# Performance work log

Measured on AMD Instinct MI355X. Metric: run time of the kernel, lower is better.

## Reference

```python
import jax, jax.numpy as jnp
import numpy as np

EPS = 1e-5

def _layer_norm(y, w, b):
    mu = y.mean(-1, keepdims=True)
    var = jnp.mean((y - mu) ** 2, axis=-1, keepdims=True)
    return (y - mu) * jax.lax.rsqrt(var + EPS) * w + b


def setup_inputs() -> dict:
    key = jax.random.key(0)
    ks = jax.random.split(key, 8)
    B, D, H, W = 1, 96, 96, 96
    N, R, K = 16, 6, 4
    x = jax.random.normal(ks[0], (B, D, H, W), jnp.float32)
    x_proj_weight = jax.random.normal(ks[1], (K, R + 2 * N, D), jnp.float32) * 0.05
    dt_projs_weight = jax.random.normal(ks[2], (K, D, R), jnp.float32) * 0.1
    dt_projs_bias = jax.random.normal(ks[3], (K, D), jnp.float32) * 0.1
    A_logs = jax.random.normal(ks[4], (K * D, N), jnp.float32)
    Ds = jax.random.normal(ks[5], (K * D,), jnp.float32) * 0.1
    ln_w = jnp.ones((D,), jnp.float32)
    ln_b = jnp.zeros((D,), jnp.float32)
    return {"x": x, "x_proj_weight": x_proj_weight, "dt_projs_weight": dt_projs_weight,
            "dt_projs_bias": dt_projs_bias, "A_logs": A_logs, "Ds": Ds,
            "ln_w": ln_w, "ln_b": ln_b}


def reference(x, x_proj_weight, dt_projs_weight, dt_projs_bias, A_logs, Ds, ln_w, ln_b):
    B, D, H, W = x.shape
    L = H * W
    K = x_proj_weight.shape[0]            # 4 scan directions
    N = A_logs.shape[1]                   # d_state
    R = dt_projs_weight.shape[2]          # dt_rank

    # ---- CrossScan: 4 directional flattenings -> xs [B, K, D, L]
    xs0 = x.reshape(B, D, L)
    xs1 = jnp.swapaxes(x, 2, 3).reshape(B, D, L)
    xs = jnp.stack([xs0, xs1, xs0[:, :, ::-1], xs1[:, :, ::-1]], axis=1)

    # ---- input-dependent projections
    x_dbl = jnp.einsum('bkdl,kcd->bkcl', xs, x_proj_weight)    # [B,K,R+2N,L]
    dts = x_dbl[:, :, :R]
    Bs = x_dbl[:, :, R:R + N]                                  # [B,K,N,L]
    Cs = x_dbl[:, :, R + N:]                                   # [B,K,N,L]
    dts = jnp.einsum('bkrl,kdr->bkdl', dts, dt_projs_weight)   # [B,K,D,L]

    # ---- selective scan (S6), delta_softplus=True, fp32
    delta = jax.nn.softplus(dts + dt_projs_bias[None, :, :, None])   # [B,K,D,L]
    A = -jnp.exp(A_logs).reshape(K, D, N)                             # [K,D,N]
    dA = jnp.exp(jnp.einsum('bkdl,kdn->bkdln', delta, A))             # [B,K,D,L,N]
    dBu = jnp.einsum('bkdl,bknl,bkdl->bkdln', delta, Bs, xs)          # delta*B*u

    def combine(c1, c2):
        a1, b1 = c1
        a2, b2 = c2
        return a1 * a2, a2 * b1 + b2

    _, h = jax.lax.associative_scan(combine, (dA, dBu), axis=3)       # h_t over L

    y = jnp.einsum('bkdln,bknl->bkdl', h, Cs)
    y = y + xs * Ds.reshape(K, D)[None, :, :, None]                   # [B,K,D,L]

    # ---- CrossMerge: undo the 4 directional scans and sum
    ys = y[:, 0:2] + y[:, 2:4, :, ::-1]                               # [B,2,D,L]
    ym = ys[:, 0] + jnp.swapaxes(ys[:, 1].reshape(B, D, W, H), 2, 3).reshape(B, D, L)

    # ---- out_norm (LayerNorm over D) and reshape to [B,H,W,D]
    yout = jnp.swapaxes(ym, 1, 2)                                     # [B,L,D]
    yout = _layer_norm(yout, ln_w, ln_b).reshape(B, H, W, D)
    return yout.astype(x.dtype)
```

## Files before the change

### kernel.cpp

```cpp
#include <hip/hip_runtime.h>
#include <math.h>

constexpr int cD = 96, cL = 9216, cK = 4;
constexpr int CL = 36, NCH = 256;
constexpr float LOG2E = 1.44269504088896f;

constexpr long OFF_XT    = 0;
constexpr long OFF_DELTA = OFF_XT    + (long)cD*cL;
constexpr long OFF_BS    = OFF_DELTA + 4L*cD*cL;
constexpr long OFF_CS    = OFF_BS    + 4L*cL*16;
constexpr long OFF_Y     = OFF_CS    + 4L*cL*16;
constexpr long OFF_SUMP  = OFF_Y     + 4L*cD*cL;
constexpr long OFF_SUMS  = OFF_SUMP  + 384L*256*16;

__device__ __forceinline__ float4 a2prep(float4 v) {
    return make_float4(-LOG2E * exp2f(LOG2E * v.x), -LOG2E * exp2f(LOG2E * v.y),
                       -LOG2E * exp2f(LOG2E * v.z), -LOG2E * exp2f(LOG2E * v.w));
}

__global__ __launch_bounds__(256) void kT(const float* __restrict__ x,
                                          float* __restrict__ xT) {
    __shared__ float t[32][33];
    const int h0 = blockIdx.x * 32, w0 = blockIdx.y * 32, d = blockIdx.z;
    const float* xd = x + (long)d * cL;
    float* xtd = xT + (long)d * cL;
    for (int o = threadIdx.x; o < 1024; o += 256) {
        int i = o >> 5, j = o & 31;
        t[i][j] = xd[(h0 + i) * 96 + w0 + j];
    }
    __syncthreads();
    for (int o = threadIdx.x; o < 1024; o += 256) {
        int i = o >> 5, j = o & 31;
        xtd[(w0 + i) * 96 + h0 + j] = t[j][i];
    }
}

__global__ __launch_bounds__(256) void kA(const float* __restrict__ x,
                                          const float* __restrict__ xT,
                                          const float* __restrict__ xpw,
                                          const float* __restrict__ dtw,
                                          const float* __restrict__ dtb,
                                          float* __restrict__ delta,
                                          float* __restrict__ Bs,
                                          float* __restrict__ Cs) {
    __shared__ float xs[96][64];
    __shared__ float xdbl[38][65];
    __shared__ float dtw_l[96 * 6];
    __shared__ float dtb_l[96];
    const int p0 = blockIdx.x * 64;
    const int k  = blockIdx.y;
    const int tid = threadIdx.x;
    const float* src = (k & 1) ? xT : x;

    for (int o = tid; o < 96 * 64; o += 256) {
        int dd = o >> 6, pp = o & 63;
        xs[dd][pp] = src[(long)dd * cL + p0 + pp];
    }
    for (int o = tid; o < 96 * 6; o += 256) dtw_l[o] = dtw[k * 96 * 6 + o];
    if (tid < 96) dtb_l[tid] = dtb[k * 96 + tid];
    __syncthreads();

    const int lane = tid & 63;
    const int c0 = __builtin_amdgcn_readfirstlane((tid >> 6) * 10);
    const float* wk = xpw + (long)k * 38 * 96;
    float acc[10];
    #pragma unroll
    for (int i = 0; i < 10; ++i) acc[i] = 0.f;
    #pragma unroll 4
    for (int dd = 0; dd < 96; ++dd) {
        float xv = xs[dd][lane];
        #pragma unroll
        for (int i = 0; i < 10; ++i) {
            int c = c0 + i; c = c > 37 ? 37 : c;
            acc[i] = fmaf(xv, wk[c * 96 + dd], acc[i]);
        }
    }
    #pragma unroll
    for (int i = 0; i < 10; ++i) {
        int c = c0 + i; c = c > 37 ? 37 : c;
        xdbl[c][lane] = acc[i];
    }
    __syncthreads();

    for (int o = tid; o < 64 * 16; o += 256) {
        int n = o & 15, pp = o >> 4;
        int P = p0 + pp;
        int q = (k < 2) ? P : (9215 - P);
        int ch = q / 36, j = q - ch * 36;
        long idx = (((long)k * 36 + j) * 256 + ch) * 16 + n;
        Bs[idx] = xdbl[6 + n][pp];
        Cs[idx] = xdbl[22 + n][pp];
    }
    for (int o = tid; o < 96 * 64; o += 256) {
        int dd = o >> 6, pp = o & 63;
        float s = dtb_l[dd];
        #pragma unroll
        for (int r = 0; r < 6; ++r) s = fmaf(xdbl[r][pp], dtw_l[dd * 6 + r], s);
        float sp = fmaxf(s, 0.f) + __logf(1.f + __expf(-fabsf(s)));
        delta[((long)(k * 96 + dd)) * cL + p0 + pp] = sp;
    }
}

template<int REV>
__device__ __forceinline__ void sum_chunk(const float* __restrict__ dB,
                                          const float* __restrict__ xB,
                                          const float* __restrict__ bB,
                                          float4 a2, float4& hO, float& sdlO) {
    float4 h = make_float4(0.f, 0.f, 0.f, 0.f);
    float sdl = 0.f;
#define S1(DL, XV, OFF) { \
        float4 B = *(const float4*)(bB + (OFF) * 4096); \
        float t = (DL) * (XV); sdl += (DL); \
        h.x = fmaf(exp2f((DL)*a2.x), h.x, t*B.x); \
        h.y = fmaf(exp2f((DL)*a2.y), h.y, t*B.y); \
        h.z = fmaf(exp2f((DL)*a2.z), h.z, t*B.z); \
        h.w = fmaf(exp2f((DL)*a2.w), h.w, t*B.w); }
    #pragma unroll
    for (int g = 0; g < 9; ++g) {
        float4 d4 = *(const float4*)(REV ? dB - 4*g - 3 : dB + 4*g);
        float4 x4 = *(const float4*)(REV ? xB - 4*g - 3 : xB + 4*g);
        if (!REV) { S1(d4.x,x4.x,4*g) S1(d4.y,x4.y,4*g+1) S1(d4.z,x4.z,4*g+2) S1(d4.w,x4.w,4*g+3) }
        else      { S1(d4.w,x4.w,4*g) S1(d4.z,x4.z,4*g+1) S1(d4.y,x4.y,4*g+2) S1(d4.x,x4.x,4*g+3) }
    }
#undef S1
    hO = h; sdlO = sdl;
}

__global__ __launch_bounds__(512, 6) void kS1(const float* __restrict__ x,
                                              const float* __restrict__ xT,
                                              const float* __restrict__ delta,
                                              const float* __restrict__ Bs,
                                              const float* __restrict__ Alog,
                                              float* __restrict__ Pg,
                                              float* __restrict__ Sg) {
    const int tid = threadIdx.x;
    const int n0 = (tid & 3) * 4, chl = tid >> 2;
    const int hb = blockIdx.x & 1, seq = blockIdx.x >> 1;
    const int k = seq / 96, d = seq % 96, rev = k >> 1;
    const int ch = hb * 128 + chl;
    const int q0 = rev ? (9215 - ch * CL) : ch * CL;

    const float4 a2 = a2prep(*(const float4*)(Alog + (long)seq * 16 + n0));
    const float* dB = delta + (long)seq * cL + q0;
    const float* xB = ((k & 1) ? xT : x) + (long)d * cL + q0;
    const float* bB = Bs + (long)k * 36 * 4096 + (long)ch * 16 + n0;

    float4 h; float sdl;
    if (!rev) sum_chunk<0>(dB, xB, bB, a2, h, sdl);
    else      sum_chunk<1>(dB, xB, bB, a2, h, sdl);

    long o = ((long)seq * NCH + ch) * 16 + n0;
    *(float4*)(Pg + o) = make_float4(exp2f(a2.x*sdl), exp2f(a2.y*sdl),
                                     exp2f(a2.z*sdl), exp2f(a2.w*sdl));
    *(float4*)(Sg + o) = h;
}

__global__ __launch_bounds__(512, 6) void kS2(const float* __restrict__ x,
                                              const float* __restrict__ xT,
                                              const float* __restrict__ delta,
                                              const float* __restrict__ Bs,
                                              const float* __restrict__ Cs,
                                              const float* __restrict__ Alog,
                                              const float* __restrict__ Dsv,
                                              const float* __restrict__ Pg,
                                              const float* __restrict__ Sg,
                                              float* __restrict__ y) {
    __shared__ float lp[NCH][16];
    __shared__ float ls[NCH][16];
    __shared__ float ybuf[4608 + 48];
    float* gpf = &lp[0][0];
    const int tid = threadIdx.x;
    const int hb = blockIdx.x & 1, seq = blockIdx.x >> 1;
    const int k = seq / 96, d = seq % 96, rev = k >> 1;

    #pragma unroll
    for (int i = 0; i < 8; ++i) {
        ((float*)lp)[tid + i * 512] = Pg[(long)seq * 4096 + tid + i * 512];
        ((float*)ls)[tid + i * 512] = Sg[(long)seq * 4096 + tid + i * 512];
    }
    __syncthreads();

    const int sn = tid & 15, sg = tid >> 4;
    float LPe[8], LSe[8];
    {
        float P = 1.f, S = 0.f;
        #pragma unroll
        for (int i = 0; i < 8; ++i) {
            LPe[i] = P; LSe[i] = S;
            float p = lp[sg * 8 + i][sn], s = ls[sg * 8 + i][sn];
            S = fmaf(p, S, s); P = p * P;
        }
        __syncthreads();
        gpf[tid] = P; gpf[512 + tid] = S;
    }
    __syncthreads();
    #pragma unroll
    for (int off = 1; off < 32; off <<= 1) {
        float pc = gpf[tid], sc = gpf[512 + tid];
        float pn = pc, snn = sc;
        if (sg >= off) {
            pn  = pc * gpf[(sg - off) * 16 + sn];
            snn = fmaf(pc, gpf[512 + (sg - off) * 16 + sn], sc);
        }
        __syncthreads();
        gpf[tid] = pn; gpf[512 + tid] = snn;
        __syncthreads();
    }
    const float GS = (sg == 0) ? 0.f : gpf[512 + (sg - 1) * 16 + sn];
    #pragma unroll
    for (int i = 0; i < 8; ++i) ls[sg * 8 + i][sn] = fmaf(LPe[i], GS, LSe[i]);
    __syncthreads();

    const int n0 = (tid & 3) * 4, chl = tid >> 2;
    const int ch = hb * 128 + chl;
    const int q0 = rev ? (9215 - ch * CL) : ch * CL;
    const float4 a2 = a2prep(*(const float4*)(Alog + (long)seq * 16 + n0));
    const float Dv = Dsv[seq];
    const float* dB = delta + (long)seq * cL + q0;
    const float* xB = ((k & 1) ? xT : x) + (long)d * cL + q0;
    const float* bB = Bs + (long)k * 36 * 4096 + (long)ch * 16 + n0;
    const float* cB = Cs + (long)k * 36 * 4096 + (long)ch * 16 + n0;
    float4 h = *(float4*)&ls[ch][n0];
    const int slB = chl * CL;
    const bool lane0 = (tid & 3) == 0;

#define S2(RV, DL, XV, OFF) { \
        float4 B = *(const float4*)(bB + (OFF) * 4096); \
        float4 C = *(const float4*)(cB + (OFF) * 4096); \
        float t = (DL) * (XV); \
        h.x = fmaf(exp2f((DL)*a2.x), h.x, t*B.x); \
        h.y = fmaf(exp2f((DL)*a2.y), h.y, t*B.y); \
        h.z = fmaf(exp2f((DL)*a2.z), h.z, t*B.z); \
        h.w = fmaf(exp2f((DL)*a2.w), h.w, t*B.w); \
        float pv = fmaf(h.x, C.x, fmaf(h.y, C.y, fmaf(h.z, C.z, h.w * C.w))); \
        pv += __shfl_xor(pv, 1, 4); \
        pv += __shfl_xor(pv, 2, 4); \
        if (lane0) { int sl = slB + (OFF); int yloc = RV ? 4607 - sl : sl; \
                     ybuf[yloc + yloc / 96] = fmaf(Dv, (XV), pv); } }
    if (!rev) {
        #pragma unroll
        for (int g = 0; g < 9; ++g) {
            float4 d4 = *(const float4*)(dB + 4*g);
            float4 x4 = *(const float4*)(xB + 4*g);
            S2(0, d4.x, x4.x, 4*g)   S2(0, d4.y, x4.y, 4*g+1)
            S2(0, d4.z, x4.z, 4*g+2) S2(0, d4.w, x4.w, 4*g+3)
        }
    } else {
        #pragma unroll
        for (int g = 0; g < 9; ++g) {
            float4 d4 = *(const float4*)(dB - 4*g - 3);
            float4 x4 = *(const float4*)(xB - 4*g - 3);
            S2(1, d4.w, x4.w, 4*g)   S2(1, d4.z, x4.z, 4*g+1)
            S2(1, d4.y, x4.y, 4*g+2) S2(1, d4.x, x4.x, 4*g+3)
        }
    }
#undef S2
    __syncthreads();

    const int sb = rev ? (1 - hb) * 4608 : hb * 4608;
    float* yrow = y + (long)seq * cL;
    if (k & 1) {
        const int w0 = sb / 96;
        for (int o = tid; o < 4608; o += 512) {
            int hh = o / 48, wl = o - hh * 48;
            yrow[hh * 96 + w0 + wl] = ybuf[wl * 97 + hh];
        }
    } else {
        for (int o = tid; o < 4608; o += 512) {
            yrow[sb + o] = ybuf[o + o / 96];
        }
    }
}

__global__ __launch_bounds__(256) void kE(const float* __restrict__ y,
                                          const float* __restrict__ lnw,
                                          const float* __restrict__ lnb,
                                          float* __restrict__ out) {
    __shared__ float vs[96][36];
    __shared__ float red[8][32], red2[8][32];
    __shared__ float MU[32], RS[32];
    const int tid = threadIdx.x;
    const int p0 = blockIdx.x * 32;

    for (int o = tid; o < 96 * 8; o += 256) {
        int dd = o >> 3, j = o & 7;
        const float* r0 = y + (long)dd * cL + p0;
        const float* r1 = y + (long)(96 + dd) * cL + p0;
        const float* r2 = y + (long)(192 + dd) * cL + p0;
        const float* r3 = y + (long)(288 + dd) * cL + p0;
        float4 a = ((const float4*)r0)[j];
        float4 b = ((const float4*)r1)[j];
        float4 c = ((const float4*)r2)[j];
        float4 e = ((const float4*)r3)[j];
        *(float4*)&vs[dd][4 * j] = make_float4(a.x + b.x + c.x + e.x,
                                               a.y + b.y + c.y + e.y,
                                               a.z + b.z + c.z + e.z,
                                               a.w + b.w + c.w + e.w);
    }
    __syncthreads();

    const int p = tid & 31, part = tid >> 5;
    float s = 0.f, s2 = 0.f;
    for (int dd = part * 12; dd < part * 12 + 12; ++dd) {
        float v = vs[dd][p];
        s += v; s2 = fmaf(v, v, s2);
    }
    red[part][p] = s; red2[part][p] = s2;
    __syncthreads();
    if (tid < 32) {
        float S = 0.f, S2 = 0.f;
        #pragma unroll
        for (int q = 0; q < 8; ++q) { S += red[q][tid]; S2 += red2[q][tid]; }
        float m = S * (1.f / 96.f);
        MU[tid] = m;
        RS[tid] = rsqrtf(S2 * (1.f / 96.f) - m * m + 1e-5f);
    }
    __syncthreads();
    for (int o = tid; o < 32 * 96; o += 256) {
        int pl = o / 96, dd = o - pl * 96;
        out[(long)(p0 + pl) * 96 + dd] = (vs[dd][pl] - MU[pl]) * RS[pl] * lnw[dd] + lnb[dd];
    }
}

extern "C" void kernel_launch(void* const* d_in, const int* in_sizes, int n_in,
                              void* d_out, int out_size, void* d_ws, size_t ws_size,
                              hipStream_t stream) {
    const float* x    = (const float*)d_in[0];
    const float* xpw  = (const float*)d_in[1];
    const float* dtw  = (const float*)d_in[2];
    const float* dtb  = (const float*)d_in[3];
    const float* Alog = (const float*)d_in[4];
    const float* Dsv  = (const float*)d_in[5];
    const float* lnw  = (const float*)d_in[6];
    const float* lnb  = (const float*)d_in[7];
    float* ws = (float*)d_ws;

    float* xT    = ws + OFF_XT;
    float* delta = ws + OFF_DELTA;
    float* Bs    = ws + OFF_BS;
    float* Cs    = ws + OFF_CS;
    float* y     = ws + OFF_Y;
    float* Pg    = ws + OFF_SUMP;
    float* Sg    = ws + OFF_SUMS;
    float* out   = (float*)d_out;

    kT<<<dim3(3, 3, 96), 256, 0, stream>>>(x, xT);
    kA<<<dim3(144, 4), 256, 0, stream>>>(x, xT, xpw, dtw, dtb, delta, Bs, Cs);
    kS1<<<768, 512, 0, stream>>>(x, xT, delta, Bs, Alog, Pg, Sg);
    kS2<<<768, 512, 0, stream>>>(x, xT, delta, Bs, Cs, Alog, Dsv, Pg, Sg, y);
    kE<<<288, 256, 0, stream>>>(y, lnw, lnb, out);
}
```

Measured before the change: 100.3 us.

## Fuse two-pass chunked scan into one kernel with one block per sequence

Merges the chunk-summary kernel and the scan/output kernel into a single kernel where each 512-thread block handles a whole (direction, channel) sequence of 9216 steps in 128 chunks of 72. Chunk summaries go straight to shared memory rather than a global workspace, which removes the extra launch and the global round trip of the partial products and sums. The cost is only 384 blocks, twice the serial chunk length, a larger shared output buffer and a lower occupancy hint, so latency hiding and SM fill may suffer.

```diff
diff --git a/kernel.cpp b/kernel.cpp
--- a/kernel.cpp
+++ b/kernel.cpp
@@ -2,7 +2,7 @@
 #include <math.h>
 
 constexpr int cD = 96, cL = 9216, cK = 4;
-constexpr int CL = 36, NCH = 256;
+constexpr int CL = 72, NCH = 128;
 constexpr float LOG2E = 1.44269504088896f;
 
 constexpr long OFF_XT    = 0;
@@ -10,8 +10,6 @@
 constexpr long OFF_BS    = OFF_DELTA + 4L*cD*cL;
 constexpr long OFF_CS    = OFF_BS    + 4L*cL*16;
 constexpr long OFF_Y     = OFF_CS    + 4L*cL*16;
-constexpr long OFF_SUMP  = OFF_Y     + 4L*cD*cL;
-constexpr long OFF_SUMS  = OFF_SUMP  + 384L*256*16;
 
 __device__ __forceinline__ float4 a2prep(float4 v) {
     return make_float4(-LOG2E * exp2f(LOG2E * v.x), -LOG2E * exp2f(LOG2E * v.y),
@@ -86,8 +84,8 @@
         int n = o & 15, pp = o >> 4;
         int P = p0 + pp;
         int q = (k < 2) ? P : (9215 - P);
-        int ch = q / 36, j = q - ch * 36;
-        long idx = (((long)k * 36 + j) * 256 + ch) * 16 + n;
+        int ch = q / 72, j = q - ch * 72;
+        long idx = (((long)k * 72 + j) * 128 + ch) * 16 + n;
         Bs[idx] = xdbl[6 + n][pp];
         Cs[idx] = xdbl[22 + n][pp];
     }
@@ -101,93 +99,71 @@
     }
 }
 
-template<int REV>
-__device__ __forceinline__ void sum_chunk(const float* __restrict__ dB,
-                                          const float* __restrict__ xB,
-                                          const float* __restrict__ bB,
-                                          float4 a2, float4& hO, float& sdlO) {
+__global__ __launch_bounds__(512, 4) void kS(const float* __restrict__ x,
+                                             const float* __restrict__ xT,
+                                             const float* __restrict__ delta,
+                                             const float* __restrict__ Bs,
+                                             const float* __restrict__ Cs,
+                                             const float* __restrict__ Alog,
+                                             const float* __restrict__ Dsv,
+                                             float* __restrict__ y) {
+    __shared__ float lp[NCH][16];
+    __shared__ float ls[NCH][16];
+    __shared__ float ybuf[9216 + 96];
+    float* gpf = &lp[0][0];
+    const int tid = threadIdx.x;
+    const int seq = blockIdx.x;
+    const int k = seq / 96, d = seq % 96, rev = k >> 1;
+    const int n0 = (tid & 3) * 4, ch = tid >> 2;
+    const int q0 = rev ? (9215 - ch * CL) : ch * CL;
+
+    const float4 a2 = a2prep(*(const float4*)(Alog + (long)seq * 16 + n0));
+    const float Dv = Dsv[seq];
+    const float* dB = delta + (long)seq * cL + q0;
+    const float* xB = ((k & 1) ? xT : x) + (long)d * cL + q0;
+    const float* bB = Bs + (long)k * cL * 16 + (long)ch * 16 + n0;
+    const float* cB = Cs + (long)k * cL * 16 + (long)ch * 16 + n0;
+
     float4 h = make_float4(0.f, 0.f, 0.f, 0.f);
     float sdl = 0.f;
 #define S1(DL, XV, OFF) { \
-        float4 B = *(const float4*)(bB + (OFF) * 4096); \
+        float4 B = *(const float4*)(bB + (OFF) * 2048); \
         float t = (DL) * (XV); sdl += (DL); \
         h.x = fmaf(exp2f((DL)*a2.x), h.x, t*B.x); \
         h.y = fmaf(exp2f((DL)*a2.y), h.y, t*B.y); \
         h.z = fmaf(exp2f((DL)*a2.z), h.z, t*B.z); \
         h.w = fmaf(exp2f((DL)*a2.w), h.w, t*B.w); }
-    #pragma unroll
-    for (int g = 0; g < 9; ++g) {
-        float4 d4 = *(const float4*)(REV ? dB - 4*g - 3 : dB + 4*g);
-        float4 x4 = *(const float4*)(REV ? xB - 4*g - 3 : xB + 4*g);
-        if (!REV) { S1(d4.x,x4.x,4*g) S1(d4.y,x4.y,4*g+1) S1(d4.z,x4.z,4*g+2) S1(d4.w,x4.w,4*g+3) }
-        else      { S1(d4.w,x4.w,4*g) S1(d4.z,x4.z,4*g+1) S1(d4.y,x4.y,4*g+2) S1(d4.x,x4.x,4*g+3) }
+    if (!rev) {
+        #pragma unroll
+        for (int g = 0; g < 18; ++g) {
+            float4 d4 = *(const float4*)(dB + 4*g);
+            float4 x4 = *(const float4*)(xB + 4*g);
+            S1(d4.x, x4.x, 4*g)   S1(d4.y, x4.y, 4*g+1)
+            S1(d4.z, x4.z, 4*g+2) S1(d4.w, x4.w, 4*g+3)
+        }
+    } else {
+        #pragma unroll
+        for (int g = 0; g < 18; ++g) {
+            float4 d4 = *(const float4*)(dB - 4*g - 3);
+            float4 x4 = *(const float4*)(xB - 4*g - 3);
+            S1(d4.w, x4.w, 4*g)   S1(d4.z, x4.z, 4*g+1)
+            S1(d4.y, x4.y, 4*g+2) S1(d4.x, x4.x, 4*g+3)
+        }
     }
 #undef S1
-    hO = h; sdlO = sdl;
-}
-
-__global__ __launch_bounds__(512, 6) void kS1(const float* __restrict__ x,
-                                              const float* __restrict__ xT,
-                                              const float* __restrict__ delta,
-                                              const float* __restrict__ Bs,
-                                              const float* __restrict__ Alog,
-                                              float* __restrict__ Pg,
-                                              float* __restrict__ Sg) {
-    const int tid = threadIdx.x;
-    const int n0 = (tid & 3) * 4, chl = tid >> 2;
-    const int hb = blockIdx.x & 1, seq = blockIdx.x >> 1;
-    const int k = seq / 96, d = seq % 96, rev = k >> 1;
-    const int ch = hb * 128 + chl;
-    const int q0 = rev ? (9215 - ch * CL) : ch * CL;
-
-    const float4 a2 = a2prep(*(const float4*)(Alog + (long)seq * 16 + n0));
-    const float* dB = delta + (long)seq * cL + q0;
-    const float* xB = ((k & 1) ? xT : x) + (long)d * cL + q0;
-    const float* bB = Bs + (long)k * 36 * 4096 + (long)ch * 16 + n0;
-
-    float4 h; float sdl;
-    if (!rev) sum_chunk<0>(dB, xB, bB, a2, h, sdl);
-    else      sum_chunk<1>(dB, xB, bB, a2, h, sdl);
-
-    long o = ((long)seq * NCH + ch) * 16 + n0;
-    *(float4*)(Pg + o) = make_float4(exp2f(a2.x*sdl), exp2f(a2.y*sdl),
-                                     exp2f(a2.z*sdl), exp2f(a2.w*sdl));
-    *(float4*)(Sg + o) = h;
-}
-
-__global__ __launch_bounds__(512, 6) void kS2(const float* __restrict__ x,
-                                              const float* __restrict__ xT,
-                                              const float* __restrict__ delta,
-                                              const float* __restrict__ Bs,
-                                              const float* __restrict__ Cs,
-                                              const float* __restrict__ Alog,
-                                              const float* __restrict__ Dsv,
-                                              const float* __restrict__ Pg,
-                                              const float* __restrict__ Sg,
-                                              float* __restrict__ y) {
-    __shared__ float lp[NCH][16];
-    __shared__ float ls[NCH][16];
-    __shared__ float ybuf[4608 + 48];
-    float* gpf = &lp[0][0];
-    const int tid = threadIdx.x;
-    const int hb = blockIdx.x & 1, seq = blockIdx.x >> 1;
-    const int k = seq / 96, d = seq % 96, rev = k >> 1;
-
-    #pragma unroll
-    for (int i = 0; i < 8; ++i) {
-        ((float*)lp)[tid + i * 512] = Pg[(long)seq * 4096 + tid + i * 512];
-        ((float*)ls)[tid + i * 512] = Sg[(long)seq * 4096 + tid + i * 512];
-    }
+    *(float4*)&lp[ch][n0] = make_float4(exp2f(a2.x*sdl), exp2f(a2.y*sdl),
+                                        exp2f(a2.z*sdl), exp2f(a2.w*sdl));
+    *(float4*)&ls[ch][n0] = h;
     __syncthreads();
 
     const int sn = tid & 15, sg = tid >> 4;
-    float LPe[8], LSe[8];
+    float LPe[4], LSe[4];
     {
         float P = 1.f, S = 0.f;
         #pragma unroll
-        for (int i = 0; i < 8; ++i) {
+        for (int i = 0; i < 4; ++i) {
             LPe[i] = P; LSe[i] = S;
-            float p = lp[sg * 8 + i][sn], s = ls[sg * 8 + i][sn];
+            float p = lp[sg * 4 + i][sn], s = ls[sg * 4 + i][sn];
             S = fmaf(p, S, s); P = p * P;
         }
         __syncthreads();
@@ -199,34 +175,24 @@
         float pc = gpf[tid], sc = gpf[512 + tid];
         float pn = pc, snn = sc;
         if (sg >= off) {
-            pn  = pc * gpf[(sg - off) * 16 + sn];
-            snn = fmaf(pc, gpf[512 + (sg - off) * 16 + sn], sc);
+            pn  = pc * gpf[tid - off * 16];
+            snn = fmaf(pc, gpf[512 + tid - off * 16], sc);
         }
         __syncthreads();
         gpf[tid] = pn; gpf[512 + tid] = snn;
         __syncthreads();
     }
-    const float GS = (sg == 0) ? 0.f : gpf[512 + (sg - 1) * 16 + sn];
+    const float GS = (sg == 0) ? 0.f : gpf[512 + tid - 16];
     #pragma unroll
-    for (int i = 0; i < 8; ++i) ls[sg * 8 + i][sn] = fmaf(LPe[i], GS, LSe[i]);
-    __syncthreads();
-
-    const int n0 = (tid & 3) * 4, chl = tid >> 2;
-    const int ch = hb * 128 + chl;
-    const int q0 = rev ? (9215 - ch * CL) : ch * CL;
-    const float4 a2 = a2prep(*(const float4*)(Alog + (long)seq * 16 + n0));
-    const float Dv = Dsv[seq];
-    const float* dB = delta + (long)seq * cL + q0;
-    const float* xB = ((k & 1) ? xT : x) + (long)d * cL + q0;
-    const float* bB = Bs + (long)k * 36 * 4096 + (long)ch * 16 + n0;
-    const float* cB = Cs + (long)k * 36 * 4096 + (long)ch * 16 + n0;
-    float4 h = *(float4*)&ls[ch][n0];
-    const int slB = chl * CL;
+    for (int i = 0; i < 4; ++i) ls[sg * 4 + i][sn] = fmaf(LPe[i], GS, LSe[i]);
+    __syncthreads();
+
+    h = *(float4*)&ls[ch][n0];
+    const int slB = ch * CL;
     const bool lane0 = (tid & 3) == 0;
-
-#define S2(RV, DL, XV, OFF) { \
-        float4 B = *(const float4*)(bB + (OFF) * 4096); \
-        float4 C = *(const float4*)(cB + (OFF) * 4096); \
+#define S2(DL, XV, OFF) { \
+        float4 B = *(const float4*)(bB + (OFF) * 2048); \
+        float4 C = *(const float4*)(cB + (OFF) * 2048); \
         float t = (DL) * (XV); \
         h.x = fmaf(exp2f((DL)*a2.x), h.x, t*B.x); \
         h.y = fmaf(exp2f((DL)*a2.y), h.y, t*B.y); \
@@ -235,39 +201,37 @@
         float pv = fmaf(h.x, C.x, fmaf(h.y, C.y, fmaf(h.z, C.z, h.w * C.w))); \
         pv += __shfl_xor(pv, 1, 4); \
         pv += __shfl_xor(pv, 2, 4); \
-        if (lane0) { int sl = slB + (OFF); int yloc = RV ? 4607 - sl : sl; \
+        if (lane0) { int sl = slB + (OFF); int yloc = rev ? 9215 - sl : sl; \
                      ybuf[yloc + yloc / 96] = fmaf(Dv, (XV), pv); } }
     if (!rev) {
         #pragma unroll
-        for (int g = 0; g < 9; ++g) {
+        for (int g = 0; g < 18; ++g) {
             float4 d4 = *(const float4*)(dB + 4*g);
             float4 x4 = *(const float4*)(xB + 4*g);
-            S2(0, d4.x, x4.x, 4*g)   S2(0, d4.y, x4.y, 4*g+1)
-            S2(0, d4.z, x4.z, 4*g+2) S2(0, d4.w, x4.w, 4*g+3)
+            S2(d4.x, x4.x, 4*g)   S2(d4.y, x4.y, 4*g+1)
+            S2(d4.z, x4.z, 4*g+2) S2(d4.w, x4.w, 4*g+3)
         }
     } else {
         #pragma unroll
-        for (int g = 0; g < 9; ++g) {
+        for (int g = 0; g < 18; ++g) {
             float4 d4 = *(const float4*)(dB - 4*g - 3);
             float4 x4 = *(const float4*)(xB - 4*g - 3);
-            S2(1, d4.w, x4.w, 4*g)   S2(1, d4.z, x4.z, 4*g+1)
-            S2(1, d4.y, x4.y, 4*g+2) S2(1, d4.x, x4.x, 4*g+3)
+            S2(d4.w, x4.w, 4*g)   S2(d4.z, x4.z, 4*g+1)
+            S2(d4.y, x4.y, 4*g+2) S2(d4.x, x4.x, 4*g+3)
         }
     }
 #undef S2
     __syncthreads();
 
-    const int sb = rev ? (1 - hb) * 4608 : hb * 4608;
     float* yrow = y + (long)seq * cL;
     if (k & 1) {
-        const int w0 = sb / 96;
-        for (int o = tid; o < 4608; o += 512) {
-            int hh = o / 48, wl = o - hh * 48;
-            yrow[hh * 96 + w0 + wl] = ybuf[wl * 97 + hh];
+        for (int o = tid; o < 9216; o += 512) {
+            int hh = o / 96, wl = o - hh * 96;
+            yrow[o] = ybuf[wl * 97 + hh];
         }
     } else {
-        for (int o = tid; o < 4608; o += 512) {
-            yrow[sb + o] = ybuf[o + o / 96];
+        for (int o = tid; o < 9216; o += 512) {
+            yrow[o] = ybuf[o + o / 96];
         }
     }
 }
@@ -340,13 +304,10 @@
     float* Bs    = ws + OFF_BS;
     float* Cs    = ws + OFF_CS;
     float* y     = ws + OFF_Y;
-    float* Pg    = ws + OFF_SUMP;
-    float* Sg    = ws + OFF_SUMS;
     float* out   = (float*)d_out;
 
     kT<<<dim3(3, 3, 96), 256, 0, stream>>>(x, xT);
     kA<<<dim3(144, 4), 256, 0, stream>>>(x, xT, xpw, dtw, dtb, delta, Bs, Cs);
-    kS1<<<768, 512, 0, stream>>>(x, xT, delta, Bs, Alog, Pg, Sg);
-    kS2<<<768, 512, 0, stream>>>(x, xT, delta, Bs, Cs, Alog, Dsv, Pg, Sg, y);
+    kS<<<cK * cD, 512, 0, stream>>>(x, xT, delta, Bs, Cs, Alog, Dsv, y);
     kE<<<288, 256, 0, stream>>>(y, lnw, lnb, out);
 }
```

New measurement: 104.6 us. +4.3%, slower.
